# Kernel optimization log

Hardware: AMD Instinct MI355X
Metric: run time of the kernel (lower is better)

## Reference

```python
import jax, jax.numpy as jnp
import numpy as np

B, S, H, DK, DV = 2, 2048, 8, 64, 192
C = H * DV          # 1536 input/output channels
KP = H * DK         # 512 key projection size
F = 192             # num_position_features (asymmetric -> 96 basis per class)


def positional_features(positions, feature_size, seq_length):
    """Central-mask relative positional features, asymmetric version.
    positions: [..., P]; returns [..., P, feature_size]."""
    nb = feature_size // 2  # num_basis_per_class (symmetric=False -> 2 components)
    pow_rate = np.exp(np.log(seq_length + 1) / nb).astype(np.float32)
    center_widths = pow_rate ** jnp.arange(1, nb + 1, dtype=jnp.float32) - 1.0  # [nb]
    emb = (center_widths > jnp.abs(positions)[..., None]).astype(jnp.float32)   # [..., P, nb]
    return jnp.concatenate([emb, jnp.sign(positions)[..., None] * emb], axis=-1)


def relative_shift(x):
    """TransformerXL relative shift: [B,H,T,2T-1] -> [B,H,T,T]."""
    b, h, t1, _ = x.shape
    x = jnp.pad(x, ((0, 0), (0, 0), (0, 0), (1, 0)))   # [B,H,T,2T]
    t2 = x.shape[-1]                                    # 2T
    x = x.reshape(b, h, t2, t1)[:, :, 1:, :]            # drop first row
    x = x.reshape(b, h, t1, t2 - 1)
    return x[..., : (t2 + 1) // 2]                      # [B,H,T,T]


def setup_inputs() -> dict:
    key = jax.random.key(0)
    ks = jax.random.split(key, 8)
    sd_in = 1.0 / np.sqrt(C)
    sd_f = 1.0 / np.sqrt(F)
    return {
        "x": jax.random.normal(ks[0], (B, S, C), jnp.float32),
        "Wq": jax.random.normal(ks[1], (C, KP), jnp.float32) * sd_in,
        "Wk": jax.random.normal(ks[2], (C, KP), jnp.float32) * sd_in,
        "Wv": jax.random.normal(ks[3], (C, C), jnp.float32) * sd_in,
        "Wr": jax.random.normal(ks[4], (F, KP), jnp.float32) * sd_f,
        "r_w_bias": jax.random.normal(ks[5], (1, H, 1, DK), jnp.float32) * 0.02,
        "r_r_bias": jax.random.normal(ks[6], (1, H, 1, DK), jnp.float32) * 0.02,
        "We": jax.random.normal(ks[7], (C, C), jnp.float32) * sd_in,
        "be": jnp.zeros((C,), jnp.float32),
    }


def reference(x, Wq, Wk, Wv, Wr, r_w_bias, r_r_bias, We, be):
    b, s, _ = x.shape

    def heads(y, d):  # [B,S,H*d] -> [B,H,S,d]
        return y.reshape(b, s, H, d).transpose(0, 2, 1, 3)

    q = heads(x @ Wq, DK) * (DK ** -0.5)
    k = heads(x @ Wk, DK)
    v = heads(x @ Wv, DV)

    distances = jnp.arange(-s + 1, s, dtype=jnp.float32)[None]      # [1, 2S-1]
    pe = positional_features(distances, F, s)                        # [1, 2S-1, F]
    r_k = (pe @ Wr).reshape(1, 2 * s - 1, H, DK).transpose(0, 2, 1, 3)[0]  # [H, 2S-1, DK]

    content_logits = jnp.einsum('bhqd,bhkd->bhqk', q + r_w_bias, k)          # [B,H,S,S]
    relative_logits = jnp.einsum('bhqd,hrd->bhqr', q + r_r_bias, r_k)        # [B,H,S,2S-1]
    logits = content_logits + relative_shift(relative_logits)

    weights = jax.nn.softmax(logits, axis=-1)
    out = jnp.einsum('bhqk,bhkd->bhqd', weights, v)                  # [B,H,S,DV]
    attended = out.transpose(0, 2, 1, 3).reshape(b, s, H * DV)       # [B,S,C]
    return attended @ We + be
```

## Files before the change

kernel.cpp:

```cpp
#include <hip/hip_runtime.h>
#include <hip/hip_bf16.h>
#include <math.h>

#define BB 2
#define SQ 2048
#define NH 8
#define DKH 64
#define DVH 192
#define CIN 1536
#define KPD 512

typedef unsigned short u16t;
typedef short bf16x8 __attribute__((ext_vector_type(8)));
typedef float f32x4 __attribute__((ext_vector_type(4)));
typedef __attribute__((address_space(3))) unsigned char lds_u8;
typedef const __attribute__((address_space(1))) unsigned char glb_u8;

__device__ __forceinline__ u16t f2bf(float f) {
    unsigned int x = __float_as_uint(f);
    unsigned int r = x + 0x7FFF + ((x >> 16) & 1);
    return (u16t)(r >> 16);
}
__device__ __forceinline__ float bf2f(u16t u) {
    return __uint_as_float(((unsigned int)u) << 16);
}
__device__ __forceinline__ void gload16(const void* g, void* l) {
    __builtin_amdgcn_global_load_lds((glb_u8*)g, (lds_u8*)l, 16, 0, 0);
}

__global__ void suffix_kernel(const float* __restrict__ Wr,
                              float* __restrict__ SUF0, float* __restrict__ SUF1) {
    int o = blockIdx.x * 256 + threadIdx.x;
    if (o >= KPD) return;
    float s = 0.f;
    SUF0[96 * KPD + o] = 0.f;
    for (int j = 95; j >= 0; j--) { s += Wr[j * KPD + o]; SUF0[j * KPD + o] = s; }
    s = 0.f;
    SUF1[96 * KPD + o] = 0.f;
    for (int j = 95; j >= 0; j--) { s += Wr[(96 + j) * KPD + o]; SUF1[j * KPD + o] = s; }
}

__global__ void jmt_kernel(unsigned char* __restrict__ jmt) {
    int tid = threadIdx.x;
    __shared__ float cwv[96];
    double pr_d = exp(log((double)(SQ + 1)) / 96.0);
    if (tid < 96) cwv[tid] = (float)(pow(pr_d, (double)(tid + 1)) - 1.0);
    __syncthreads();
    for (int dist = tid; dist < SQ; dist += 256) {
        float ad = (float)dist;
        int jm = 0;
        for (int j = 0; j < 96; j++) jm += (cwv[j] <= ad) ? 1 : 0;
        jmt[dist] = (unsigned char)jm;
    }
}

__global__ void conv_x(const float* __restrict__ x, u16t* __restrict__ xhi,
                       u16t* __restrict__ xlo) {
    size_t i = ((size_t)blockIdx.x * 256 + threadIdx.x) * 8;
    float4 a = *(const float4*)(x + i), b4 = *(const float4*)(x + i + 4);
    float v[8] = {a.x, a.y, a.z, a.w, b4.x, b4.y, b4.z, b4.w};
    u16t hi[8], lo[8];
#pragma unroll
    for (int j = 0; j < 8; j++) {
        hi[j] = f2bf(v[j]);
        lo[j] = f2bf(v[j] - bf2f(hi[j]));
    }
    ushort4 h0 = {hi[0], hi[1], hi[2], hi[3]}, h1 = {hi[4], hi[5], hi[6], hi[7]};
    ushort4 l0 = {lo[0], lo[1], lo[2], lo[3]}, l1 = {lo[4], lo[5], lo[6], lo[7]};
    *(ushort4*)&xhi[i] = h0; *(ushort4*)&xhi[i + 4] = h1;
    *(ushort4*)&xlo[i] = l0; *(ushort4*)&xlo[i + 4] = l1;
}

__global__ __launch_bounds__(256) void tconv(
    const float* __restrict__ src, u16t* __restrict__ dhi, u16t* __restrict__ dlo, int N) {
    __shared__ float tile[64][65];
    const int k0 = blockIdx.y * 64, n0 = blockIdx.x * 64;
    const int t = threadIdx.x;
    const int lr = t >> 4, lc4 = (t & 15) * 4;
#pragma unroll
    for (int rep = 0; rep < 4; rep++) {
        int row = rep * 16 + lr;
        *(float4*)&tile[row][lc4] = *(const float4*)(src + (size_t)(k0 + row) * N + n0 + lc4);
    }
    __syncthreads();
    const int nl = t >> 2, ks = t & 3;
    u16t hi[16], lo[16];
#pragma unroll
    for (int j = 0; j < 16; j++) {
        float v = tile[ks * 16 + j][nl];
        hi[j] = f2bf(v); lo[j] = f2bf(v - bf2f(hi[j]));
    }
    size_t off = (size_t)(n0 + nl) * CIN + k0 + ks * 16;
#pragma unroll
    for (int j = 0; j < 4; j++) {
        ushort4 h = {hi[4 * j], hi[4 * j + 1], hi[4 * j + 2], hi[4 * j + 3]};
        ushort4 lo4 = {lo[4 * j], lo[4 * j + 1], lo[4 * j + 2], lo[4 * j + 3]};
        *(ushort4*)&dhi[off + 4 * j] = h;
        *(ushort4*)&dlo[off + 4 * j] = lo4;
    }
}

__global__ __launch_bounds__(256) void a01_kernel(
    const float* __restrict__ Q, const float* __restrict__ SUF0,
    const float* __restrict__ SUF1, const float* __restrict__ rrb,
    unsigned int* __restrict__ A01) {
    __shared__ float s0[97][65];
    __shared__ float s1[97][65];
    __shared__ float qs[32][65];
    int h = blockIdx.y, b = blockIdx.z, qb = blockIdx.x * 32;
    int tid = threadIdx.x;
    for (int idx = tid; idx < 97 * 64; idx += 256) {
        int j = idx >> 6, e = idx & 63;
        s0[j][e] = SUF0[j * KPD + h * 64 + e];
        s1[j][e] = SUF1[j * KPD + h * 64 + e];
    }
    for (int idx = tid; idx < 32 * 64; idx += 256) {
        int q = idx >> 6, e = idx & 63;
        qs[q][e] = Q[((size_t)(b * SQ + qb + q)) * KPD + h * 64 + e] + rrb[h * 64 + e];
    }
    __syncthreads();
    int q = tid >> 3, part = tid & 7;
    for (int j = part; j < 97; j += 8) {
        float d0 = 0.f, d1 = 0.f;
        for (int e = 0; e < 64; e++) {
            float qv = qs[q][e];
            d0 += qv * s0[j][e];
            d1 += qv * s1[j][e];
        }
        unsigned int pk = ((unsigned int)f2bf(d1) << 16) | (unsigned int)f2bf(d0);
        A01[(((size_t)(b * NH + h)) * SQ + qb + q) * 97 + j] = pk;
    }
}

__device__ __forceinline__ void gemm3_core(
    const u16t* __restrict__ Ahi, const u16t* __restrict__ Alo,
    const u16t* __restrict__ Bhi, const u16t* __restrict__ Blo,
    u16t* lds, f32x4 (&acc)[4][4]) {
    const int tid = threadIdx.x;
    const int w = tid >> 6, l = tid & 63;
    const int lan15 = l & 15, grp = l >> 4;
    const int wr = w >> 1, wc = w & 1;

#pragma unroll
    for (int a = 0; a < 4; a++)
#pragma unroll
        for (int bq = 0; bq < 4; bq++) acc[a][bq] = (f32x4){0.f, 0.f, 0.f, 0.f};

    const u16t* gsrc = (w == 0) ? Ahi : (w == 1) ? Alo : (w == 2) ? Bhi : Blo;
    const int srow = l >> 2, sc = (l & 3) * 8;
    u16t* lbase = lds + w * 4096;

    for (int kt = 0; kt < 48; kt++) {
        const int k0 = kt * 32;
#pragma unroll
        for (int j = 0; j < 8; j++) {
            int row = j * 16 + srow;
            gload16(gsrc + (size_t)row * CIN + k0 + sc, lbase + j * 512);
        }
        __syncthreads();
        bf16x8 ah[4], al[4], bh[4], bl[4];
#pragma unroll
        for (int mi = 0; mi < 4; mi++) {
            int row = wr * 64 + mi * 16 + lan15;
            ah[mi] = *(const bf16x8*)&lds[row * 32 + grp * 8];
            al[mi] = *(const bf16x8*)&lds[4096 + row * 32 + grp * 8];
        }
#pragma unroll
        for (int ni = 0; ni < 4; ni++) {
            int row = wc * 64 + ni * 16 + lan15;
            bh[ni] = *(const bf16x8*)&lds[8192 + row * 32 + grp * 8];
            bl[ni] = *(const bf16x8*)&lds[12288 + row * 32 + grp * 8];
        }
#pragma unroll
        for (int mi = 0; mi < 4; mi++)
#pragma unroll
            for (int ni = 0; ni < 4; ni++) {
                acc[mi][ni] = __builtin_amdgcn_mfma_f32_16x16x32_bf16(ah[mi], bh[ni], acc[mi][ni], 0, 0, 0);
                acc[mi][ni] = __builtin_amdgcn_mfma_f32_16x16x32_bf16(ah[mi], bl[ni], acc[mi][ni], 0, 0, 0);
                acc[mi][ni] = __builtin_amdgcn_mfma_f32_16x16x32_bf16(al[mi], bh[ni], acc[mi][ni], 0, 0, 0);
            }
        __syncthreads();
    }
}

__global__ __launch_bounds__(256) void qkv_gemm3(
    const u16t* __restrict__ XAhi, const u16t* __restrict__ XAlo,
    const u16t* __restrict__ Whi, const u16t* __restrict__ Wlo,
    float* __restrict__ Q, u16t* __restrict__ Kbf, u16t* __restrict__ VT) {
    __shared__ __align__(16) u16t lds[16384];
    const int n0 = blockIdx.x * 128, m0 = blockIdx.y * 128;
    f32x4 acc[4][4];
    gemm3_core(XAhi + (size_t)m0 * CIN, XAlo + (size_t)m0 * CIN,
               Whi + (size_t)n0 * CIN, Wlo + (size_t)n0 * CIN, lds, acc);
    const int tid = threadIdx.x, w = tid >> 6, l = tid & 63;
    const int lan15 = l & 15, grp = l >> 4, wr = w >> 1, wc = w & 1;
    if (n0 < 512) {
#pragma unroll
        for (int mi = 0; mi < 4; mi++)
#pragma unroll
            for (int ni = 0; ni < 4; ni++) {
                int gn = n0 + wc * 64 + ni * 16 + lan15;
                int gm0 = m0 + wr * 64 + mi * 16 + grp * 4;
#pragma unroll
                for (int i = 0; i < 4; i++)
                    Q[(size_t)(gm0 + i) * KPD + gn] = acc[mi][ni][i] * 0.125f;
            }
    } else if (n0 < 1024) {
#pragma unroll
        for (int mi = 0; mi < 4; mi++)
#pragma unroll
            for (int ni = 0; ni < 4; ni++) {
                int gn = n0 - 512 + wc * 64 + ni * 16 + lan15;
                int gm0 = m0 + wr * 64 + mi * 16 + grp * 4;
#pragma unroll
                for (int i = 0; i < 4; i++)
                    Kbf[(size_t)(gm0 + i) * KPD + gn] = f2bf(acc[mi][ni][i]);
            }
    } else {
#pragma unroll
        for (int mi = 0; mi < 4; mi++)
#pragma unroll
            for (int ni = 0; ni < 4; ni++) {
                int cv = n0 - 1024 + wc * 64 + ni * 16 + lan15;
                int hh = cv / 192, dv = cv - hh * 192;
                int gm0 = m0 + wr * 64 + mi * 16 + grp * 4;
                int bidx = gm0 >> 11, s = gm0 & 2047;
                ushort4 pk = {f2bf(acc[mi][ni][0]), f2bf(acc[mi][ni][1]),
                              f2bf(acc[mi][ni][2]), f2bf(acc[mi][ni][3])};
                *(ushort4*)&VT[((size_t)(bidx * NH + hh) * 192 + dv) * SQ + s] = pk;
            }
    }
}

__global__ __launch_bounds__(256) void out_gemm3(
    const u16t* __restrict__ Ahi, const u16t* __restrict__ Alo,
    const u16t* __restrict__ Whi, const u16t* __restrict__ Wlo,
    const float* __restrict__ be, float* __restrict__ out) {
    __shared__ __align__(16) u16t lds[16384];
    const int n0 = blockIdx.x * 128, m0 = blockIdx.y * 128;
    f32x4 acc[4][4];
    gemm3_core(Ahi + (size_t)m0 * CIN, Alo + (size_t)m0 * CIN,
               Whi + (size_t)n0 * CIN, Wlo + (size_t)n0 * CIN, lds, acc);
    const int tid = threadIdx.x, w = tid >> 6, l = tid & 63;
    const int lan15 = l & 15, grp = l >> 4, wr = w >> 1, wc = w & 1;
#pragma unroll
    for (int mi = 0; mi < 4; mi++)
#pragma unroll
        for (int ni = 0; ni < 4; ni++) {
            int gn = n0 + wc * 64 + ni * 16 + lan15;
            int gm0 = m0 + wr * 64 + mi * 16 + grp * 4;
            float bev = be[gn];
#pragma unroll
            for (int i = 0; i < 4; i++)
                out[(size_t)(gm0 + i) * CIN + gn] = acc[mi][ni][i] + bev;
        }
}

__global__ void ck_kernel(const u16t* __restrict__ Kbf, const float* __restrict__ rwb,
                          float* __restrict__ cK) {
    int g = blockIdx.x * 256 + threadIdx.x;
    int k = g & 2047, h = (g >> 11) & 7, b = g >> 14;
    const u16t* kp = Kbf + ((size_t)(b * SQ + k)) * KPD + h * 64;
    const float* wp = rwb + h * 64;
    float s = 0.f;
#pragma unroll
    for (int c = 0; c < 8; c++) {
        bf16x8 kv = *(const bf16x8*)(kp + c * 8);
#pragma unroll
        for (int j = 0; j < 8; j++) s += bf2f((u16t)kv[j]) * wp[c * 8 + j];
    }
    cK[g] = s;
}

__global__ __launch_bounds__(256) void attn_mfma(
    const float* __restrict__ Q, const u16t* __restrict__ Kbf, const u16t* __restrict__ VT,
    const unsigned int* __restrict__ A01, const unsigned char* __restrict__ jmtg,
    const float* __restrict__ cKg, u16t* __restrict__ ATThi, u16t* __restrict__ ATTlo) {
    __shared__ __align__(16) u16t k_s[32 * 72];
    __shared__ __align__(16) u16t vt_s[192 * 40];
    __shared__ __align__(16) u16t p_s[4][16 * 40];
    __shared__ unsigned int a01_s[64 * 97];
    __shared__ unsigned char jmt_s[2048];
    __shared__ float ck_s[32];

    const int q0blk = blockIdx.x * 64;
    const int h = blockIdx.y, b = blockIdx.z;
    const int tid = threadIdx.x;
    const int w = tid >> 6, l = tid & 63;
    const int lan15 = l & 15, grp = l >> 4;

    ((uint2*)jmt_s)[tid] = ((const uint2*)jmtg)[tid];
    {
        const unsigned int* a01g = A01 + (((size_t)(b * NH + h)) * SQ + q0blk) * 97;
        for (int idx = tid; idx < 64 * 97; idx += 256) a01_s[idx] = a01g[idx];
    }

    const int qrow = q0blk + w * 16 + lan15;
    bf16x8 qfrag[2];
#pragma unroll
    for (int g = 0; g < 2; g++) {
        const float* qp = Q + ((size_t)(b * SQ + qrow)) * KPD + h * 64 + g * 32 + grp * 8;
        float4 qa = *(const float4*)qp, qb4 = *(const float4*)(qp + 4);
        bf16x8 f;
        f[0] = (short)f2bf(qa.x); f[1] = (short)f2bf(qa.y);
        f[2] = (short)f2bf(qa.z); f[3] = (short)f2bf(qa.w);
        f[4] = (short)f2bf(qb4.x); f[5] = (short)f2bf(qb4.y);
        f[6] = (short)f2bf(qb4.z); f[7] = (short)f2bf(qb4.w);
        qfrag[g] = f;
    }

    f32x4 o_acc[12];
#pragma unroll
    for (int c = 0; c < 12; c++) o_acc[c] = (f32x4){0.f, 0.f, 0.f, 0.f};
    float m_run[4] = {-INFINITY, -INFINITY, -INFINITY, -INFINITY};
    float l_run[4] = {0.f, 0.f, 0.f, 0.f};

    const u16t* Kbase = Kbf + ((size_t)b * SQ) * KPD + h * 64;
    const u16t* Vbase = VT + ((size_t)(b * NH + h)) * 192 * SQ;
    const float* cKb = cKg + (size_t)(b * NH + h) * SQ;
    u16t* p_ws = p_s[w];

    for (int kt = 0; kt < SQ / 32; kt++) {
        const int k0 = kt * 32;
        {
            int row = tid >> 3, g = tid & 7;
            *(bf16x8*)&k_s[row * 72 + g * 8] =
                *(const bf16x8*)(Kbase + (size_t)(k0 + row) * KPD + g * 8);
        }
#pragma unroll
        for (int rep = 0; rep < 3; rep++) {
            int c = tid + rep * 256;
            int dv = c >> 2, g = c & 3;
            *(bf16x8*)&vt_s[dv * 40 + g * 8] =
                *(const bf16x8*)(Vbase + (size_t)dv * SQ + k0 + g * 8);
        }
        if (tid < 32) ck_s[tid] = cKb[k0 + tid];
        __syncthreads();

        f32x4 sacc[2];
#pragma unroll
        for (int ct = 0; ct < 2; ct++) {
            int krow = 16 * ct + lan15;
            bf16x8 kf0 = *(bf16x8*)&k_s[krow * 72 + grp * 8];
            bf16x8 kf1 = *(bf16x8*)&k_s[krow * 72 + 32 + grp * 8];
            f32x4 z = (f32x4){0.f, 0.f, 0.f, 0.f};
            z = __builtin_amdgcn_mfma_f32_16x16x32_bf16(qfrag[0], kf0, z, 0, 0, 0);
            z = __builtin_amdgcn_mfma_f32_16x16x32_bf16(qfrag[1], kf1, z, 0, 0, 0);
            sacc[ct] = z;
        }
        float ckv[2] = {ck_s[lan15], ck_s[16 + lan15]};

#pragma unroll
        for (int i = 0; i < 4; i++) {
            const int qg = q0blk + w * 16 + grp * 4 + i;
            float sv[2];
#pragma unroll
            for (int ct = 0; ct < 2; ct++) {
                int kg = k0 + 16 * ct + lan15;
                int dg = kg - qg;
                int dist = dg < 0 ? -dg : dg;
                int jm = (int)jmt_s[dist];
                unsigned int pk = a01_s[(w * 16 + grp * 4 + i) * 97 + jm];
                float a0 = bf2f((u16t)(pk & 0xFFFF));
                float a1 = bf2f((u16t)(pk >> 16));
                float sgn = (dg > 0) ? 1.f : (dg < 0 ? -1.f : 0.f);
                sv[ct] = sacc[ct][i] + a0 + sgn * a1 + ckv[ct];
            }
            float mx = fmaxf(sv[0], sv[1]);
            mx = fmaxf(mx, __shfl_xor(mx, 1));
            mx = fmaxf(mx, __shfl_xor(mx, 2));
            mx = fmaxf(mx, __shfl_xor(mx, 4));
            mx = fmaxf(mx, __shfl_xor(mx, 8));
            float mn = fmaxf(m_run[i], mx);
            float scl = __expf(m_run[i] - mn);
            float p0 = __expf(sv[0] - mn), p1 = __expf(sv[1] - mn);
            float ls = p0 + p1;
            ls += __shfl_xor(ls, 1);
            ls += __shfl_xor(ls, 2);
            ls += __shfl_xor(ls, 4);
            ls += __shfl_xor(ls, 8);
            l_run[i] = l_run[i] * scl + ls;
            m_run[i] = mn;
#pragma unroll
            for (int c = 0; c < 12; c++) o_acc[c][i] *= scl;
            p_ws[(grp * 4 + i) * 40 + lan15]      = f2bf(p0);
            p_ws[(grp * 4 + i) * 40 + 16 + lan15] = f2bf(p1);
        }

        bf16x8 pa = *(bf16x8*)&p_ws[lan15 * 40 + grp * 8];
#pragma unroll
        for (int c = 0; c < 12; c++) {
            bf16x8 vf = *(bf16x8*)&vt_s[(16 * c + lan15) * 40 + grp * 8];
            o_acc[c] = __builtin_amdgcn_mfma_f32_16x16x32_bf16(pa, vf, o_acc[c], 0, 0, 0);
        }
        __syncthreads();
    }

    float inv[4];
#pragma unroll
    for (int i = 0; i < 4; i++) inv[i] = 1.f / l_run[i];
#pragma unroll
    for (int c = 0; c < 12; c++)
#pragma unroll
        for (int i = 0; i < 4; i++) {
            int qg = q0blk + w * 16 + grp * 4 + i;
            size_t idx = ((size_t)(b * SQ + qg)) * CIN + h * 192 + 16 * c + lan15;
            float o = o_acc[c][i] * inv[i];
            u16t hv = f2bf(o);
            ATThi[idx] = hv;
            ATTlo[idx] = f2bf(o - bf2f(hv));
        }
}

extern "C" void kernel_launch(void* const* d_in, const int* in_sizes, int n_in,
                              void* d_out, int out_size, void* d_ws, size_t ws_size,
                              hipStream_t stream) {
    const float* x   = (const float*)d_in[0];
    const float* Wq  = (const float*)d_in[1];
    const float* Wk  = (const float*)d_in[2];
    const float* Wv  = (const float*)d_in[3];
    const float* Wr  = (const float*)d_in[4];
    const float* rwb = (const float*)d_in[5];
    const float* rrb = (const float*)d_in[6];
    const float* We  = (const float*)d_in[7];
    const float* be  = (const float*)d_in[8];
    float* out = (float*)d_out;

    float* ws = (float*)d_ws;
    float* Q     = ws;
    u16t*  Kbf   = (u16t*)(ws + 2097152);
    u16t*  VT    = (u16t*)(ws + 3145728);
    u16t*  XAhi  = (u16t*)(ws + 6291456);
    u16t*  XAlo  = (u16t*)(ws + 9437184);
    u16t*  WTh   = (u16t*)(ws + 12582912);
    u16t*  WTl   = (u16t*)(ws + 14548992);
    float* SUF0  = ws + 16515072;
    float* SUF1  = ws + 16564736;
    float* cKb   = ws + 16614400;
    unsigned char* jmt = (unsigned char*)(ws + 16647168);
    unsigned int* A01  = (unsigned int*)(ws + 12582912);
    u16t*  WeTh  = (u16t*)(ws);
    u16t*  WeTl  = (u16t*)(ws + 1179648);

    suffix_kernel<<<2, 256, 0, stream>>>(Wr, SUF0, SUF1);
    jmt_kernel<<<1, 256, 0, stream>>>(jmt);
    conv_x<<<3072, 256, 0, stream>>>(x, XAhi, XAlo);
    tconv<<<dim3(8, 24), 256, 0, stream>>>(Wq, WTh, WTl, KPD);
    tconv<<<dim3(8, 24), 256, 0, stream>>>(Wk, WTh + (size_t)512 * CIN, WTl + (size_t)512 * CIN, KPD);
    tconv<<<dim3(24, 24), 256, 0, stream>>>(Wv, WTh + (size_t)1024 * CIN, WTl + (size_t)1024 * CIN, CIN);
    qkv_gemm3<<<dim3(20, 32), 256, 0, stream>>>(XAhi, XAlo, WTh, WTl, Q, Kbf, VT);
    ck_kernel<<<128, 256, 0, stream>>>(Kbf, rwb, cKb);
    a01_kernel<<<dim3(64, NH, BB), 256, 0, stream>>>(Q, SUF0, SUF1, rrb, A01);
    attn_mfma<<<dim3(SQ / 64, NH, BB), 256, 0, stream>>>(Q, Kbf, VT, A01, jmt, cKb, XAhi, XAlo);
    tconv<<<dim3(24, 24), 256, 0, stream>>>(We, WeTh, WeTl, CIN);
    out_gemm3<<<dim3(12, 32), 256, 0, stream>>>(XAhi, XAlo, WeTh, WeTl, be, out);
}
```

Baseline: 619.6 us.

## Fold content bias into Q, pre-combine relative terms, load K/V directly

Adds r_w_bias into the Q fragment before the QK MFMA, which removes the separate ck_kernel and its per-key bias term. The a01 table now stores precombined (a0+a1) and (a0-a1) values, so the inner loop selects one half by sign instead of doing a multiply-add. The attention loop widens key tiles from 32 to 64 and reads K and V fragments straight from global memory instead of staging them through LDS. This cuts LDS traffic and one kernel launch, but the kernel now relies on L2/cache for K/V reuse across the four waves and does more uncoalesced global loads.

```diff
diff --git a/kernel.cpp b/kernel.cpp
--- a/kernel.cpp
+++ b/kernel.cpp
@@ -127,7 +127,9 @@
             d0 += qv * s0[j][e];
             d1 += qv * s1[j][e];
         }
-        unsigned int pk = ((unsigned int)f2bf(d1) << 16) | (unsigned int)f2bf(d0);
+        float pos = (j == 0) ? d0 : (d0 + d1);
+        float neg = (j == 0) ? d0 : (d0 - d1);
+        unsigned int pk = ((unsigned int)f2bf(pos) << 16) | (unsigned int)f2bf(neg);
         A01[(((size_t)(b * NH + h)) * SQ + qb + q) * 97 + j] = pk;
     }
 }
@@ -256,32 +258,13 @@
         }
 }
 
-__global__ void ck_kernel(const u16t* __restrict__ Kbf, const float* __restrict__ rwb,
-                          float* __restrict__ cK) {
-    int g = blockIdx.x * 256 + threadIdx.x;
-    int k = g & 2047, h = (g >> 11) & 7, b = g >> 14;
-    const u16t* kp = Kbf + ((size_t)(b * SQ + k)) * KPD + h * 64;
-    const float* wp = rwb + h * 64;
-    float s = 0.f;
-#pragma unroll
-    for (int c = 0; c < 8; c++) {
-        bf16x8 kv = *(const bf16x8*)(kp + c * 8);
-#pragma unroll
-        for (int j = 0; j < 8; j++) s += bf2f((u16t)kv[j]) * wp[c * 8 + j];
-    }
-    cK[g] = s;
-}
-
 __global__ __launch_bounds__(256) void attn_mfma(
     const float* __restrict__ Q, const u16t* __restrict__ Kbf, const u16t* __restrict__ VT,
     const unsigned int* __restrict__ A01, const unsigned char* __restrict__ jmtg,
-    const float* __restrict__ cKg, u16t* __restrict__ ATThi, u16t* __restrict__ ATTlo) {
-    __shared__ __align__(16) u16t k_s[32 * 72];
-    __shared__ __align__(16) u16t vt_s[192 * 40];
-    __shared__ __align__(16) u16t p_s[4][16 * 40];
+    const float* __restrict__ rwb, u16t* __restrict__ ATThi, u16t* __restrict__ ATTlo) {
     __shared__ unsigned int a01_s[64 * 97];
     __shared__ unsigned char jmt_s[2048];
-    __shared__ float ck_s[32];
+    __shared__ __align__(16) u16t p_s[4][16 * 72];
 
     const int q0blk = blockIdx.x * 64;
     const int h = blockIdx.y, b = blockIdx.z;
@@ -300,12 +283,14 @@
 #pragma unroll
     for (int g = 0; g < 2; g++) {
         const float* qp = Q + ((size_t)(b * SQ + qrow)) * KPD + h * 64 + g * 32 + grp * 8;
+        const float* wp = rwb + h * 64 + g * 32 + grp * 8;
         float4 qa = *(const float4*)qp, qb4 = *(const float4*)(qp + 4);
+        float4 wa = *(const float4*)wp, wb4 = *(const float4*)(wp + 4);
         bf16x8 f;
-        f[0] = (short)f2bf(qa.x); f[1] = (short)f2bf(qa.y);
-        f[2] = (short)f2bf(qa.z); f[3] = (short)f2bf(qa.w);
-        f[4] = (short)f2bf(qb4.x); f[5] = (short)f2bf(qb4.y);
-        f[6] = (short)f2bf(qb4.z); f[7] = (short)f2bf(qb4.w);
+        f[0] = (short)f2bf(qa.x + wa.x); f[1] = (short)f2bf(qa.y + wa.y);
+        f[2] = (short)f2bf(qa.z + wa.z); f[3] = (short)f2bf(qa.w + wa.w);
+        f[4] = (short)f2bf(qb4.x + wb4.x); f[5] = (short)f2bf(qb4.y + wb4.y);
+        f[6] = (short)f2bf(qb4.z + wb4.z); f[7] = (short)f2bf(qb4.w + wb4.w);
         qfrag[g] = f;
     }
 
@@ -317,56 +302,40 @@
 
     const u16t* Kbase = Kbf + ((size_t)b * SQ) * KPD + h * 64;
     const u16t* Vbase = VT + ((size_t)(b * NH + h)) * 192 * SQ;
-    const float* cKb = cKg + (size_t)(b * NH + h) * SQ;
     u16t* p_ws = p_s[w];
 
-    for (int kt = 0; kt < SQ / 32; kt++) {
-        const int k0 = kt * 32;
-        {
-            int row = tid >> 3, g = tid & 7;
-            *(bf16x8*)&k_s[row * 72 + g * 8] =
-                *(const bf16x8*)(Kbase + (size_t)(k0 + row) * KPD + g * 8);
-        }
-#pragma unroll
-        for (int rep = 0; rep < 3; rep++) {
-            int c = tid + rep * 256;
-            int dv = c >> 2, g = c & 3;
-            *(bf16x8*)&vt_s[dv * 40 + g * 8] =
-                *(const bf16x8*)(Vbase + (size_t)dv * SQ + k0 + g * 8);
-        }
-        if (tid < 32) ck_s[tid] = cKb[k0 + tid];
-        __syncthreads();
-
-        f32x4 sacc[2];
-#pragma unroll
-        for (int ct = 0; ct < 2; ct++) {
-            int krow = 16 * ct + lan15;
-            bf16x8 kf0 = *(bf16x8*)&k_s[krow * 72 + grp * 8];
-            bf16x8 kf1 = *(bf16x8*)&k_s[krow * 72 + 32 + grp * 8];
+    __syncthreads();
+
+    for (int kt = 0; kt < SQ / 64; kt++) {
+        const int k0 = kt * 64;
+
+        f32x4 sacc[4];
+#pragma unroll
+        for (int ct = 0; ct < 4; ct++) {
+            const u16t* kp = Kbase + (size_t)(k0 + 16 * ct + lan15) * KPD + grp * 8;
+            bf16x8 kf0 = *(const bf16x8*)kp;
+            bf16x8 kf1 = *(const bf16x8*)(kp + 32);
             f32x4 z = (f32x4){0.f, 0.f, 0.f, 0.f};
             z = __builtin_amdgcn_mfma_f32_16x16x32_bf16(qfrag[0], kf0, z, 0, 0, 0);
             z = __builtin_amdgcn_mfma_f32_16x16x32_bf16(qfrag[1], kf1, z, 0, 0, 0);
             sacc[ct] = z;
         }
-        float ckv[2] = {ck_s[lan15], ck_s[16 + lan15]};
 
 #pragma unroll
         for (int i = 0; i < 4; i++) {
             const int qg = q0blk + w * 16 + grp * 4 + i;
-            float sv[2];
-#pragma unroll
-            for (int ct = 0; ct < 2; ct++) {
+            const int arow = (w * 16 + grp * 4 + i) * 97;
+            float sv[4];
+#pragma unroll
+            for (int ct = 0; ct < 4; ct++) {
                 int kg = k0 + 16 * ct + lan15;
                 int dg = kg - qg;
                 int dist = dg < 0 ? -dg : dg;
-                int jm = (int)jmt_s[dist];
-                unsigned int pk = a01_s[(w * 16 + grp * 4 + i) * 97 + jm];
-                float a0 = bf2f((u16t)(pk & 0xFFFF));
-                float a1 = bf2f((u16t)(pk >> 16));
-                float sgn = (dg > 0) ? 1.f : (dg < 0 ? -1.f : 0.f);
-                sv[ct] = sacc[ct][i] + a0 + sgn * a1 + ckv[ct];
+                unsigned int pk = a01_s[arow + (int)jmt_s[dist]];
+                u16t hf = (dg >= 0) ? (u16t)(pk >> 16) : (u16t)(pk & 0xFFFF);
+                sv[ct] = sacc[ct][i] + bf2f(hf);
             }
-            float mx = fmaxf(sv[0], sv[1]);
+            float mx = fmaxf(fmaxf(sv[0], sv[1]), fmaxf(sv[2], sv[3]));
             mx = fmaxf(mx, __shfl_xor(mx, 1));
             mx = fmaxf(mx, __shfl_xor(mx, 2));
             mx = fmaxf(mx, __shfl_xor(mx, 4));
@@ -374,7 +343,8 @@
             float mn = fmaxf(m_run[i], mx);
             float scl = __expf(m_run[i] - mn);
             float p0 = __expf(sv[0] - mn), p1 = __expf(sv[1] - mn);
-            float ls = p0 + p1;
+            float p2 = __expf(sv[2] - mn), p3 = __expf(sv[3] - mn);
+            float ls = (p0 + p1) + (p2 + p3);
             ls += __shfl_xor(ls, 1);
             ls += __shfl_xor(ls, 2);
             ls += __shfl_xor(ls, 4);
@@ -383,16 +353,26 @@
             m_run[i] = mn;
 #pragma unroll
             for (int c = 0; c < 12; c++) o_acc[c][i] *= scl;
-            p_ws[(grp * 4 + i) * 40 + lan15]      = f2bf(p0);
-            p_ws[(grp * 4 + i) * 40 + 16 + lan15] = f2bf(p1);
-        }
-
-        bf16x8 pa = *(bf16x8*)&p_ws[lan15 * 40 + grp * 8];
+            const int prow = (grp * 4 + i) * 72;
+            p_ws[prow + lan15]      = f2bf(p0);
+            p_ws[prow + 16 + lan15] = f2bf(p1);
+            p_ws[prow + 32 + lan15] = f2bf(p2);
+            p_ws[prow + 48 + lan15] = f2bf(p3);
+        }
+
+        __syncthreads();
+
+        bf16x8 pa0 = *(bf16x8*)&p_ws[lan15 * 72 + grp * 8];
+        bf16x8 pa1 = *(bf16x8*)&p_ws[lan15 * 72 + 32 + grp * 8];
 #pragma unroll
         for (int c = 0; c < 12; c++) {
-            bf16x8 vf = *(bf16x8*)&vt_s[(16 * c + lan15) * 40 + grp * 8];
-            o_acc[c] = __builtin_amdgcn_mfma_f32_16x16x32_bf16(pa, vf, o_acc[c], 0, 0, 0);
-        }
+            const u16t* vp = Vbase + (size_t)(16 * c + lan15) * SQ + k0 + grp * 8;
+            bf16x8 vf0 = *(const bf16x8*)vp;
+            bf16x8 vf1 = *(const bf16x8*)(vp + 32);
+            o_acc[c] = __builtin_amdgcn_mfma_f32_16x16x32_bf16(pa0, vf0, o_acc[c], 0, 0, 0);
+            o_acc[c] = __builtin_amdgcn_mfma_f32_16x16x32_bf16(pa1, vf1, o_acc[c], 0, 0, 0);
+        }
+
         __syncthreads();
     }
 
@@ -436,8 +416,7 @@
     u16t*  WTl   = (u16t*)(ws + 14548992);
     float* SUF0  = ws + 16515072;
     float* SUF1  = ws + 16564736;
-    float* cKb   = ws + 16614400;
-    unsigned char* jmt = (unsigned char*)(ws + 16647168);
+    unsigned char* jmt = (unsigned char*)(ws + 16614400);
     unsigned int* A01  = (unsigned int*)(ws + 12582912);
     u16t*  WeTh  = (u16t*)(ws);
     u16t*  WeTl  = (u16t*)(ws + 1179648);
@@ -449,9 +428,8 @@
     tconv<<<dim3(8, 24), 256, 0, stream>>>(Wk, WTh + (size_t)512 * CIN, WTl + (size_t)512 * CIN, KPD);
     tconv<<<dim3(24, 24), 256, 0, stream>>>(Wv, WTh + (size_t)1024 * CIN, WTl + (size_t)1024 * CIN, CIN);
     qkv_gemm3<<<dim3(20, 32), 256, 0, stream>>>(XAhi, XAlo, WTh, WTl, Q, Kbf, VT);
-    ck_kernel<<<128, 256, 0, stream>>>(Kbf, rwb, cKb);
     a01_kernel<<<dim3(64, NH, BB), 256, 0, stream>>>(Q, SUF0, SUF1, rrb, A01);
-    attn_mfma<<<dim3(SQ / 64, NH, BB), 256, 0, stream>>>(Q, Kbf, VT, A01, jmt, cKb, XAhi, XAlo);
+    attn_mfma<<<dim3(SQ / 64, NH, BB), 256, 0, stream>>>(Q, Kbf, VT, A01, jmt, rwb, XAhi, XAlo);
     tconv<<<dim3(24, 24), 256, 0, stream>>>(We, WeTh, WeTl, CIN);
     out_gemm3<<<dim3(12, 32), 256, 0, stream>>>(XAhi, XAlo, WeTh, WeTl, be, out);
 }
```

Result: slower. 741.9 us (+19.7%).
